# Kernel tuning notes

Measured on AMD Instinct MI355X. Metric: run time of the kernel, lower is better.

The kernel has to match this reference:

```python
import jax, jax.numpy as jnp
import numpy as np

V = 50257  # vocab_size
E = 512    # embed_dim
H = 512    # hidden_dim
N = 32     # batch
T = 128    # sequence length


def setup_inputs() -> dict:
    key = jax.random.key(0)
    ks = jax.random.split(key, 8)
    s = 1.0 / np.sqrt(H)  # PyTorch GRUCell init range
    words = jax.random.randint(ks[0], (N, T), 0, V)
    hidden_state = jnp.zeros((N, H), jnp.float32)
    embed_W = jax.random.uniform(ks[1], (V, E), jnp.float32, -1.0, 1.0)  # init_weights uniform_(-1,1)
    W_ih = jax.random.uniform(ks[2], (3 * H, E), jnp.float32, -s, s)
    W_hh = jax.random.uniform(ks[3], (3 * H, H), jnp.float32, -s, s)
    b_ih = jax.random.uniform(ks[4], (3 * H,), jnp.float32, -s, s)
    b_hh = jax.random.uniform(ks[5], (3 * H,), jnp.float32, -s, s)
    emit_W = jax.random.uniform(ks[6], (V, H), jnp.float32, -1.0, 1.0)
    emit_b = jnp.zeros((V,), jnp.float32)
    return {"words": words, "hidden_state": hidden_state, "embed_W": embed_W,
            "W_ih": W_ih, "W_hh": W_hh, "b_ih": b_ih, "b_hh": b_hh,
            "emit_W": emit_W, "emit_b": emit_b}


def _gru_cell(x, h, W_ih, W_hh, b_ih, b_hh):
    gi = x @ W_ih.T + b_ih          # [N, 3H]
    gh = h @ W_hh.T + b_hh          # [N, 3H]
    i_r, i_z, i_n = jnp.split(gi, 3, axis=-1)
    h_r, h_z, h_n = jnp.split(gh, 3, axis=-1)
    r = jax.nn.sigmoid(i_r + h_r)
    z = jax.nn.sigmoid(i_z + h_z)
    n = jnp.tanh(i_n + r * h_n)
    return (1.0 - z) * n + z * h


def reference(words, hidden_state, embed_W, W_ih, W_hh, b_ih, b_hh, emit_W, emit_b):
    emb = embed_W[words[:, :-1]]        # [N, T-1, E]
    xs = jnp.swapaxes(emb, 0, 1)        # [T-1, N, E]
    targets = words[:, 1:].T            # [T-1, N]

    def step(h, inp):
        x, widx = inp
        h_new = _gru_cell(x, h, W_ih, W_hh, b_ih, b_hh)
        logits = h_new @ emit_W.T + emit_b                 # [N, V]
        logp = jax.nn.log_softmax(logits, axis=-1)
        ll = jnp.take_along_axis(logp, widx[:, None], axis=1)[:, 0]  # [N]
        return h_new, ll

    h_final, lls = jax.lax.scan(step, hidden_state, (xs, targets))
    emit_marginal = lls.sum(axis=0) / (T - 1)              # [N]
    return emit_marginal, h_final
```

## Files before the change

kernel.cpp:

```cpp
#include <hip/hip_runtime.h>
#include <math.h>

#define V_SIZE 50257
#define EMB 512
#define HID 512
#define NB 32
#define TT 128
#define NSTEP 127
#define G3H 1536
#define MROWS 4064
#define MPAD 4096
#define VPAD 50304
#define NT_V 393
#define NBLK_GRU 32
#define NTILE (16 * NT_V)
#define NWORKER 448
#define SMEM_BYTES 77312

typedef __attribute__((ext_vector_type(4))) float f32x4;
typedef __attribute__((ext_vector_type(8))) __bf16 bf16x8;
typedef __attribute__((ext_vector_type(4))) __bf16 bf16x4;

struct u128 { unsigned long long a, b; };

__device__ __forceinline__ void async16(const __bf16* g, __bf16* l) {
    __builtin_amdgcn_global_load_lds(
        (const __attribute__((address_space(1))) void*)g,
        (__attribute__((address_space(3))) void*)l, 16, 0, 0);
}


__global__ void k_prep_emit(const float* __restrict__ src, __bf16* __restrict__ dst) {
    size_t total4 = (size_t)VPAD * 512 / 4;
    size_t real4  = (size_t)V_SIZE * 512 / 4;
    for (size_t i4 = (size_t)blockIdx.x * blockDim.x + threadIdx.x; i4 < total4;
         i4 += (size_t)gridDim.x * blockDim.x) {
        float4 v = (i4 < real4) ? ((const float4*)src)[i4] : make_float4(0.f,0.f,0.f,0.f);
        bf16x4 o = {(__bf16)v.x, (__bf16)v.y, (__bf16)v.z, (__bf16)v.w};
        ((bf16x4*)dst)[i4] = o;
    }
}

__global__ void k_prep_wih(const float* __restrict__ src, __bf16* __restrict__ dst) {
    size_t total4 = (size_t)G3H * 512 / 4;
    for (size_t i4 = (size_t)blockIdx.x * blockDim.x + threadIdx.x; i4 < total4;
         i4 += (size_t)gridDim.x * blockDim.x) {
        float4 v = ((const float4*)src)[i4];
        bf16x4 o = {(__bf16)v.x, (__bf16)v.y, (__bf16)v.z, (__bf16)v.w};
        ((bf16x4*)dst)[i4] = o;
    }
}

__global__ void k_prep_x(const int* __restrict__ words, const float* __restrict__ embed,
                         __bf16* __restrict__ Xb, __bf16* __restrict__ Hs) {
    int s = blockIdx.x;
    int n = blockIdx.y;
    int tid = threadIdx.x;
    if (s < NSTEP) {
        int w = words[n * TT + s];
        size_t row = (size_t)(s * NB + n);
        const float4* src = (const float4*)(embed + (size_t)w * EMB);
        bf16x4* dst = (bf16x4*)(Xb + row * EMB);
        for (int c = tid; c < EMB / 4; c += 128) {
            float4 v = src[c];
            bf16x4 o = {(__bf16)v.x, (__bf16)v.y, (__bf16)v.z, (__bf16)v.w};
            dst[c] = o;
        }
    } else {
        size_t row = (size_t)(MROWS + n);
        bf16x4 z = {(__bf16)0.f, (__bf16)0.f, (__bf16)0.f, (__bf16)0.f};
        for (int c = tid; c < EMB / 4; c += 128) {
            ((bf16x4*)(Xb + row * EMB))[c] = z;
            ((bf16x4*)(Hs + row * HID))[c] = z;
        }
    }
}

__global__ void k_prep_h0(const float* __restrict__ h0, __bf16* __restrict__ Hbuf,
                          int* __restrict__ ctrl) {
    int b = blockIdx.x;
    if (b < NB) {
        for (int k = threadIdx.x; k < HID; k += 256)
            Hbuf[b * HID + k] = (__bf16)h0[b * HID + k];
    } else {
        for (int k = threadIdx.x; k < 2048; k += 256) ctrl[k] = 0;
    }
}


__device__ __forceinline__ void mm128(const __bf16* __restrict__ A,
                                      const __bf16* __restrict__ B,
                                      int mBase, int nBase, f32x4 acc[4][4],
                                      __bf16* As, __bf16* Bs) {
    const int tid = threadIdx.x;
    const int lane = tid & 63, wave = tid >> 6;
    const int wm = wave >> 1, wn = wave & 1;
    const int lane15 = lane & 15, quad = lane >> 4;
    for (int kc = 0; kc < 512; kc += 64) {
        __syncthreads();
#pragma unroll
        for (int i = 0; i < 4; ++i) {
            int c = (wave * 4 + i) * 64 + lane;
            int row = c >> 3, ci = c & 7;
            int cis = ci ^ (row & 7);
            async16(A + (size_t)(mBase + row) * 512 + kc + (cis << 3), As + (wave * 4 + i) * 512);
            async16(B + (size_t)(nBase + row) * 512 + kc + (cis << 3), Bs + (wave * 4 + i) * 512);
        }
        __syncthreads();
#pragma unroll
        for (int ks = 0; ks < 64; ks += 32) {
            bf16x8 a4[4], b4[4];
#pragma unroll
            for (int mi = 0; mi < 4; ++mi) {
                int row = wm * 64 + mi * 16 + lane15;
                int L = (ks >> 3) + quad;
                a4[mi] = *(const bf16x8*)(As + row * 64 + ((L ^ (row & 7)) << 3));
            }
#pragma unroll
            for (int ni = 0; ni < 4; ++ni) {
                int row = wn * 64 + ni * 16 + lane15;
                int L = (ks >> 3) + quad;
                b4[ni] = *(const bf16x8*)(Bs + row * 64 + ((L ^ (row & 7)) << 3));
            }
#pragma unroll
            for (int mi = 0; mi < 4; ++mi)
#pragma unroll
                for (int ni = 0; ni < 4; ++ni)
                    acc[mi][ni] = __builtin_amdgcn_mfma_f32_16x16x32_bf16(
                        a4[mi], b4[ni], acc[mi][ni], 0, 0, 0);
        }
    }
}

__global__ __launch_bounds__(256) void k_gemm_gi(const __bf16* __restrict__ Xb,
                                                 const __bf16* __restrict__ Wihb,
                                                 const float* __restrict__ b_ih,
                                                 const float* __restrict__ b_hh,
                                                 float* __restrict__ gi) {
    __shared__ __align__(16) __bf16 As[128 * 64];
    __shared__ __align__(16) __bf16 Bs[128 * 64];
    f32x4 acc[4][4];
    f32x4 z = {0.f, 0.f, 0.f, 0.f};
#pragma unroll
    for (int mi = 0; mi < 4; ++mi)
#pragma unroll
        for (int ni = 0; ni < 4; ++ni) acc[mi][ni] = z;
    int mBase = blockIdx.x * 128, nBase = blockIdx.y * 128;
    mm128(Xb, Wihb, mBase, nBase, acc, As, Bs);
    const int tid = threadIdx.x, lane = tid & 63, wave = tid >> 6;
    const int wm = wave >> 1, wn = wave & 1, lane15 = lane & 15, quad = lane >> 4;
#pragma unroll
    for (int ni = 0; ni < 4; ++ni) {
        int col = nBase + wn * 64 + ni * 16 + lane15;
        float bias = b_ih[col] + (col < 1024 ? b_hh[col] : 0.0f);
#pragma unroll
        for (int mi = 0; mi < 4; ++mi) {
            int rowb = wm * 64 + mi * 16 + quad * 4;
#pragma unroll
            for (int r = 0; r < 4; ++r) {
                int m = mBase + rowb + r;
                gi[(size_t)m * G3H + col] = acc[mi][ni][r] + bias;
            }
        }
    }
}

#define CREDp(w,g,m,jc) Cred[(((w)*3+(g))*32+(m))*17+(jc)]

__global__ __launch_bounds__(256, 2) void k_fused(
    const float* __restrict__ W_hh, const float* __restrict__ gi,
    const float* __restrict__ b_hh, const float* __restrict__ h0,
    __bf16* __restrict__ Hbuf,
    __bf16* __restrict__ Hs,
    float* __restrict__ Hfin,
    const __bf16* __restrict__ Wemb,
    const float* __restrict__ emit_b,
    float2* __restrict__ partials,
    int* __restrict__ ctrl)
{
    __shared__ __align__(16) char smem[SMEM_BYTES];
    __shared__ int tShare;
    const int tid = threadIdx.x;
    const int lane = tid & 63, wave = tid >> 6;
    const int lane15 = lane & 15, quad = lane >> 4;
    int* ticket = ctrl;
    int* flags  = ctrl + 32;
    int* prog   = ctrl + 64;

    if (blockIdx.x < NBLK_GRU) {
        const int blk = blockIdx.x;
        const int j0 = blk * 16;
        __bf16* Wl  = (__bf16*)smem;
        float* Cred = (float*)(smem + 49920);
        __bf16 (*HbO)[16] = (__bf16(*)[16])(smem + 76032);

        for (int idx = tid; idx < 48 * 128; idx += 256) {
            int rr = idx >> 7, k4 = (idx & 127) << 2;
            int g = rr >> 4, jc = rr & 15;
            float4 v = *(const float4*)(W_hh + (size_t)(g * 512 + j0 + jc) * 512 + k4);
            __bf16* d = &Wl[rr * 520 + k4];
            d[0] = (__bf16)v.x; d[1] = (__bf16)v.y; d[2] = (__bf16)v.z; d[3] = (__bf16)v.w;
        }

        const int m0 = tid >> 4, jc0 = tid & 15;
        const int m1 = m0 + 16;
        const float bhn = b_hh[1024 + j0 + jc0];
        const int k0 = wave * 128;
        float hp0 = h0[(size_t)m0 * HID + j0 + jc0];
        float hp1 = h0[(size_t)m1 * HID + j0 + jc0];

        float ir0, iz0, in0, ir1, iz1, in1;
        {
            const float* g0 = gi + (size_t)m0 * G3H + j0 + jc0;
            const float* g1 = gi + (size_t)m1 * G3H + j0 + jc0;
            ir0 = g0[0]; iz0 = g0[512]; in0 = g0[1024];
            ir1 = g1[0]; iz1 = g1[512]; in1 = g1[1024];
        }
        __syncthreads();

        for (int s = 0; s < NSTEP; ++s) {
            const __bf16* hb = Hbuf + (size_t)(s & 1) * NB * HID;
            unsigned long long hq[2][4][2];
#pragma unroll
            for (int mt = 0; mt < 2; ++mt)
#pragma unroll
                for (int kk = 0; kk < 4; ++kk) {
                    const unsigned long long* pp = (const unsigned long long*)
                        (hb + (size_t)(mt * 16 + lane15) * HID + k0 + kk * 32 + quad * 8);
                    hq[mt][kk][0] = __hip_atomic_load(pp, __ATOMIC_RELAXED, __HIP_MEMORY_SCOPE_AGENT);
                    hq[mt][kk][1] = __hip_atomic_load(pp + 1, __ATOMIC_RELAXED, __HIP_MEMORY_SCOPE_AGENT);
                }

            f32x4 acc[2][3];
            f32x4 zz = {0.f, 0.f, 0.f, 0.f};
#pragma unroll
            for (int mt = 0; mt < 2; ++mt)
#pragma unroll
                for (int g = 0; g < 3; ++g) acc[mt][g] = zz;
#pragma unroll
            for (int kk = 0; kk < 4; ++kk) {
                int ks = kk * 32;
                bf16x8 a0 = __builtin_bit_cast(bf16x8, u128{hq[0][kk][0], hq[0][kk][1]});
                bf16x8 a1 = __builtin_bit_cast(bf16x8, u128{hq[1][kk][0], hq[1][kk][1]});
#pragma unroll
                for (int g = 0; g < 3; ++g) {
                    bf16x8 b4 = *(const bf16x8*)(&Wl[(g * 16 + lane15) * 520 + k0 + ks + quad * 8]);
                    acc[0][g] = __builtin_amdgcn_mfma_f32_16x16x32_bf16(a0, b4, acc[0][g], 0, 0, 0);
                    acc[1][g] = __builtin_amdgcn_mfma_f32_16x16x32_bf16(a1, b4, acc[1][g], 0, 0, 0);
                }
            }
#pragma unroll
            for (int mt = 0; mt < 2; ++mt)
#pragma unroll
                for (int g = 0; g < 3; ++g)
#pragma unroll
                    for (int r = 0; r < 4; ++r)
                        CREDp(wave, g, mt * 16 + quad * 4 + r, lane15) = acc[mt][g][r];
            __syncthreads();

            {
                float gr = CREDp(0,0,m0,jc0) + CREDp(1,0,m0,jc0) + CREDp(2,0,m0,jc0) + CREDp(3,0,m0,jc0);
                float gz = CREDp(0,1,m0,jc0) + CREDp(1,1,m0,jc0) + CREDp(2,1,m0,jc0) + CREDp(3,1,m0,jc0);
                float gn = CREDp(0,2,m0,jc0) + CREDp(1,2,m0,jc0) + CREDp(2,2,m0,jc0) + CREDp(3,2,m0,jc0);
                float r = 1.f / (1.f + expf(-(ir0 + gr)));
                float zg = 1.f / (1.f + expf(-(iz0 + gz)));
                float nn = tanhf(in0 + r * (gn + bhn));
                hp0 = (1.f - zg) * nn + zg * hp0;
                HbO[m0][jc0] = (__bf16)hp0;
            }
            {
                float gr = CREDp(0,0,m1,jc0) + CREDp(1,0,m1,jc0) + CREDp(2,0,m1,jc0) + CREDp(3,0,m1,jc0);
                float gz = CREDp(0,1,m1,jc0) + CREDp(1,1,m1,jc0) + CREDp(2,1,m1,jc0) + CREDp(3,1,m1,jc0);
                float gn = CREDp(0,2,m1,jc0) + CREDp(1,2,m1,jc0) + CREDp(2,2,m1,jc0) + CREDp(3,2,m1,jc0);
                float r = 1.f / (1.f + expf(-(ir1 + gr)));
                float zg = 1.f / (1.f + expf(-(iz1 + gz)));
                float nn = tanhf(in1 + r * (gn + bhn));
                hp1 = (1.f - zg) * nn + zg * hp1;
                HbO[m1][jc0] = (__bf16)hp1;
            }
            __syncthreads();

            if (tid < 128) {
                int m = tid >> 2, g4 = tid & 3;
                unsigned long long v0 = *(const unsigned short*)&HbO[m][g4 * 4 + 0];
                unsigned long long v1 = *(const unsigned short*)&HbO[m][g4 * 4 + 1];
                unsigned long long v2 = *(const unsigned short*)&HbO[m][g4 * 4 + 2];
                unsigned long long v3 = *(const unsigned short*)&HbO[m][g4 * 4 + 3];
                unsigned long long pk = v0 | (v1 << 16) | (v2 << 32) | (v3 << 48);
                unsigned long long* dst = (unsigned long long*)
                    (Hbuf + (size_t)((s + 1) & 1) * NB * HID + (size_t)m * HID + j0 + g4 * 4);
                __hip_atomic_store(dst, pk, __ATOMIC_RELAXED, __HIP_MEMORY_SCOPE_AGENT);
                unsigned long long* dst2 = (unsigned long long*)
                    (Hs + (size_t)(s * NB + m) * HID + j0 + g4 * 4);
                __hip_atomic_store(dst2, pk, __ATOMIC_RELAXED, __HIP_MEMORY_SCOPE_AGENT);
            }

            __builtin_amdgcn_s_waitcnt(0x0f70);
            __syncthreads();

            if (tid == 0)
                __hip_atomic_store(&flags[blk], s + 1,
                                   __ATOMIC_RELAXED, __HIP_MEMORY_SCOPE_AGENT);

            float nir0, niz0, nin0, nir1, niz1, nin1;
            if (s + 1 < NSTEP) {
                const float* g0 = gi + (size_t)((s + 1) * NB + m0) * G3H + j0 + jc0;
                const float* g1 = gi + (size_t)((s + 1) * NB + m1) * G3H + j0 + jc0;
                nir0 = g0[0]; niz0 = g0[512]; nin0 = g0[1024];
                nir1 = g1[0]; niz1 = g1[512]; nin1 = g1[1024];
            } else {
                nir0 = niz0 = nin0 = nir1 = niz1 = nin1 = 0.f;
            }

            if (wave == 0) {
                for (;;) {
                    int f = __hip_atomic_load(&flags[lane & 31], __ATOMIC_RELAXED,
                                              __HIP_MEMORY_SCOPE_AGENT);
                    if (__all(f >= s + 1)) break;
                    __builtin_amdgcn_s_sleep(1);
                }
            }
            __syncthreads();

            if (blk == 0 && tid < 8)
                __hip_atomic_store(&prog[tid << 5], s + 1,
                                   __ATOMIC_RELAXED, __HIP_MEMORY_SCOPE_AGENT);

            ir0 = nir0; iz0 = niz0; in0 = nin0;
            ir1 = nir1; iz1 = niz1; in1 = nin1;
        }

        Hfin[(size_t)m0 * HID + j0 + jc0] = hp0;
        Hfin[(size_t)m1 * HID + j0 + jc0] = hp1;

    } else {
        __bf16* As = (__bf16*)smem;
        __bf16* Bs = (__bf16*)(smem + 32768);
        int* myprog = prog + ((blockIdx.x & 7) << 5);
        const float NINF = -__builtin_inff();

        for (;;) {
            if (tid == 0) {
                int t = __hip_atomic_fetch_add(ticket, 1, __ATOMIC_RELAXED,
                                               __HIP_MEMORY_SCOPE_AGENT);
                tShare = t;
                if (t < NTILE) {
                    int mc = t / NT_V;
                    int need = (mc == 15) ? NSTEP : 8 * (mc + 1);
                    while (__hip_atomic_load(myprog, __ATOMIC_RELAXED,
                                             __HIP_MEMORY_SCOPE_AGENT) < need)
                        __builtin_amdgcn_s_sleep(32);
                }
            }
            __syncthreads();
            int t = tShare;
            if (t >= NTILE) break;
            int mc = t / NT_V;
            int nT = t - mc * NT_V;
            int mBase = mc * 256, nBase = nT * 128;

            f32x4 acc[4][8];
            f32x4 z = {0.f, 0.f, 0.f, 0.f};
#pragma unroll
            for (int mi = 0; mi < 4; ++mi)
#pragma unroll
                for (int ni = 0; ni < 8; ++ni) acc[mi][ni] = z;

            for (int kc = 0; kc < 512; kc += 64) {
                __syncthreads();
#pragma unroll
                for (int i = 0; i < 8; ++i) {
                    int c = (wave * 8 + i) * 64 + lane;
                    int row = c >> 3, ci = c & 7;
                    int cis = ci ^ (row & 7);
                    async16(Hs + (size_t)(mBase + row) * 512 + kc + (cis << 3),
                            As + (wave * 8 + i) * 512);
                }
#pragma unroll
                for (int i = 0; i < 4; ++i) {
                    int c = (wave * 4 + i) * 64 + lane;
                    int row = c >> 3, ci = c & 7;
                    int cis = ci ^ (row & 7);
                    async16(Wemb + (size_t)(nBase + row) * 512 + kc + (cis << 3),
                            Bs + (wave * 4 + i) * 512);
                }
                __syncthreads();
#pragma unroll
                for (int ks = 0; ks < 64; ks += 32) {
                    int L = (ks >> 3) + quad;
                    bf16x8 a4[4], b4[8];
#pragma unroll
                    for (int mi = 0; mi < 4; ++mi) {
                        int row = wave * 64 + mi * 16 + lane15;
                        a4[mi] = *(const bf16x8*)(As + row * 64 + ((L ^ (row & 7)) << 3));
                    }
#pragma unroll
                    for (int ni = 0; ni < 8; ++ni) {
                        int row = ni * 16 + lane15;
                        b4[ni] = *(const bf16x8*)(Bs + row * 64 + ((L ^ (row & 7)) << 3));
                    }
#pragma unroll
                    for (int mi = 0; mi < 4; ++mi)
#pragma unroll
                        for (int ni = 0; ni < 8; ++ni)
                            acc[mi][ni] = __builtin_amdgcn_mfma_f32_16x16x32_bf16(
                                a4[mi], b4[ni], acc[mi][ni], 0, 0, 0);
                }
            }

            float bv[8];
            bool valid[8];
#pragma unroll
            for (int ni = 0; ni < 8; ++ni) {
                int col = nBase + ni * 16 + lane15;
                valid[ni] = (col < V_SIZE);
                bv[ni] = valid[ni] ? emit_b[col] : 0.0f;
            }
#pragma unroll
            for (int mi = 0; mi < 4; ++mi) {
#pragma unroll
                for (int r = 0; r < 4; ++r) {
                    float vals[8];
                    float vmax = NINF;
#pragma unroll
                    for (int ni = 0; ni < 8; ++ni) {
                        float v = acc[mi][ni][r] + bv[ni];
                        if (!valid[ni]) v = NINF;
                        vals[ni] = v;
                        vmax = fmaxf(vmax, v);
                    }
#pragma unroll
                    for (int off = 1; off < 16; off <<= 1)
                        vmax = fmaxf(vmax, __shfl_xor(vmax, off));
                    float ssum = 0.f;
#pragma unroll
                    for (int ni = 0; ni < 8; ++ni) ssum += expf(vals[ni] - vmax);
#pragma unroll
                    for (int off = 1; off < 16; off <<= 1) ssum += __shfl_xor(ssum, off);
                    if (lane15 == 0) {
                        int m = mBase + wave * 64 + mi * 16 + quad * 4 + r;
                        partials[(size_t)m * NT_V + nT] = make_float2(vmax, ssum);
                    }
                }
            }
        }
    }
}

__global__ __launch_bounds__(128) void k_row_ll(const float2* __restrict__ partials,
                                                const __bf16* __restrict__ Hs,
                                                const __bf16* __restrict__ Wemb,
                                                const float* __restrict__ emit_b,
                                                const int* __restrict__ words,
                                                float* __restrict__ lls) {
    int s = blockIdx.x, n = blockIdx.y;
    int m = s * NB + n;
    int tid = threadIdx.x;
    int lane = tid & 63, w = tid >> 6;
    __shared__ float sm[2], ss[2], sd[2];
    const float2* prow = partials + (size_t)m * NT_V;
    float M = -__builtin_inff();
    for (int i = tid; i < NT_V; i += 128) M = fmaxf(M, prow[i].x);
#pragma unroll
    for (int off = 1; off < 64; off <<= 1) M = fmaxf(M, __shfl_xor(M, off));
    if (lane == 0) sm[w] = M;
    __syncthreads();
    M = fmaxf(sm[0], sm[1]);
    float S = 0.f;
    for (int i = tid; i < NT_V; i += 128) {
        float2 p = prow[i];
        S += p.y * expf(p.x - M);
    }
#pragma unroll
    for (int off = 1; off < 64; off <<= 1) S += __shfl_xor(S, off);
    if (lane == 0) ss[w] = S;
    __syncthreads();
    S = ss[0] + ss[1];
    int tw = words[n * TT + s + 1];
    float d = 0.f;
    const __bf16* hr = Hs + (size_t)m * HID;
    const __bf16* wr = Wemb + (size_t)tw * HID;
    for (int k = tid; k < HID; k += 128) d += (float)hr[k] * (float)wr[k];
#pragma unroll
    for (int off = 1; off < 64; off <<= 1) d += __shfl_xor(d, off);
    if (lane == 0) sd[w] = d;
    __syncthreads();
    if (tid == 0) {
        float dt = sd[0] + sd[1];
        lls[m] = dt + emit_b[tw] - (M + logf(S));
    }
}

__global__ __launch_bounds__(128) void k_final(const float* __restrict__ lls,
                                               const float* __restrict__ Hfin,
                                               float* __restrict__ out) {
    int n = blockIdx.x;
    int tid = threadIdx.x;
    float s = 0.f;
    for (int i = tid; i < NSTEP; i += 128) s += lls[i * NB + n];
#pragma unroll
    for (int off = 1; off < 64; off <<= 1) s += __shfl_xor(s, off);
    __shared__ float t2[2];
    if ((tid & 63) == 0) t2[tid >> 6] = s;
    __syncthreads();
    if (tid == 0) out[n] = (t2[0] + t2[1]) / (float)NSTEP;
    for (int i = tid; i < HID; i += 128) out[NB + n * HID + i] = Hfin[(size_t)n * HID + i];
}

extern "C" void kernel_launch(void* const* d_in, const int* in_sizes, int n_in,
                              void* d_out, int out_size, void* d_ws, size_t ws_size,
                              hipStream_t stream) {
    const int*   words   = (const int*)d_in[0];
    const float* hidden0 = (const float*)d_in[1];
    const float* embed_W = (const float*)d_in[2];
    const float* W_ih    = (const float*)d_in[3];
    const float* W_hh    = (const float*)d_in[4];
    const float* b_ih    = (const float*)d_in[5];
    const float* b_hh    = (const float*)d_in[6];
    const float* emit_W  = (const float*)d_in[7];
    const float* emit_b  = (const float*)d_in[8];
    float* out = (float*)d_out;

    char* p = (char*)d_ws;
    auto alloc = [&](size_t bytes) {
        void* r = (void*)p;
        p += (bytes + 255) & ~(size_t)255;
        return r;
    };
    __bf16* emit_Wb = (__bf16*)alloc((size_t)VPAD * 512 * 2);
    __bf16* Xb      = (__bf16*)alloc((size_t)MPAD * 512 * 2);
    __bf16* Wihb    = (__bf16*)alloc((size_t)G3H * 512 * 2);
    float*  gi      = (float*)alloc((size_t)MPAD * G3H * 4);
    __bf16* Hs      = (__bf16*)alloc((size_t)MPAD * 512 * 2);
    __bf16* Hbuf    = (__bf16*)alloc((size_t)2 * NB * HID * 2);
    float*  Hfin    = (float*)alloc((size_t)NB * HID * 4);
    float2* partials= (float2*)alloc((size_t)MPAD * NT_V * 8);
    float*  lls     = (float*)alloc((size_t)MROWS * 4);
    int*    ctrl    = (int*)alloc(2048 * 4);

    k_prep_emit<<<4096, 256, 0, stream>>>(emit_W, emit_Wb);
    k_prep_x<<<dim3(128, 32), 128, 0, stream>>>(words, embed_W, Xb, Hs);
    k_prep_wih<<<768, 256, 0, stream>>>(W_ih, Wihb);
    k_prep_h0<<<NB + 1, 256, 0, stream>>>(hidden0, Hbuf, ctrl);

    k_gemm_gi<<<dim3(32, 12), 256, 0, stream>>>(Xb, Wihb, b_ih, b_hh, gi);

    k_fused<<<NBLK_GRU + NWORKER, 256, 0, stream>>>(
        W_hh, gi, b_hh, hidden0, Hbuf, Hs, Hfin, emit_Wb, emit_b, partials, ctrl);

    k_row_ll<<<dim3(NSTEP, 32), 128, 0, stream>>>(partials, Hs, emit_Wb, emit_b, words, lls);
    k_final<<<32, 128, 0, stream>>>(lls, Hfin, out);
}
```

Before: 898.2 us.

## Merge four prep kernels into one launch and shrink fused worker count

Combines the emit-weight, W_ih, embedding-gather and h0/ctrl prep kernels into a single kernel that dispatches on block index, removing three launches and their serialization gaps. Separately, the number of worker blocks in the fused GRU+emit kernel drops from 448 to 128, which changes how the vocab-tile work is split against the GRU recurrence blocks. Fewer workers may cut contention with the recurrence blocks or the cost of spinning on flags, but gives less parallelism for the large emit GEMM.

After: 1.302 ms. +45.0%, slower.

```diff
diff --git a/kernel.cpp b/kernel.cpp
--- a/kernel.cpp
+++ b/kernel.cpp
@@ -14,7 +14,7 @@
 #define NT_V 393
 #define NBLK_GRU 32
 #define NTILE (16 * NT_V)
-#define NWORKER 448
+#define NWORKER 128
 #define SMEM_BYTES 77312
 
 typedef __attribute__((ext_vector_type(4))) float f32x4;
@@ -29,61 +29,61 @@
         (__attribute__((address_space(3))) void*)l, 16, 0, 0);
 }
 
-
-__global__ void k_prep_emit(const float* __restrict__ src, __bf16* __restrict__ dst) {
-    size_t total4 = (size_t)VPAD * 512 / 4;
-    size_t real4  = (size_t)V_SIZE * 512 / 4;
-    for (size_t i4 = (size_t)blockIdx.x * blockDim.x + threadIdx.x; i4 < total4;
-         i4 += (size_t)gridDim.x * blockDim.x) {
-        float4 v = (i4 < real4) ? ((const float4*)src)[i4] : make_float4(0.f,0.f,0.f,0.f);
+#define PREP_EMIT_BLKS 4096
+#define PREP_WIH_BLKS 768
+#define PREP_X_BLKS 128
+#define PREP_GRID (PREP_EMIT_BLKS + PREP_WIH_BLKS + PREP_X_BLKS + NB + 1)
+
+__global__ __launch_bounds__(256) void k_prep(
+    const int* __restrict__ words, const float* __restrict__ embed,
+    const float* __restrict__ emit_W, const float* __restrict__ W_ih,
+    const float* __restrict__ h0,
+    __bf16* __restrict__ emit_Wb, __bf16* __restrict__ Wihb,
+    __bf16* __restrict__ Xb, __bf16* __restrict__ Hs,
+    __bf16* __restrict__ Hbuf, int* __restrict__ ctrl)
+{
+    int b = blockIdx.x;
+    int tid = threadIdx.x;
+    if (b < PREP_EMIT_BLKS) {
+        size_t total4 = (size_t)VPAD * 512 / 4;
+        size_t real4  = (size_t)V_SIZE * 512 / 4;
+        for (size_t i4 = (size_t)b * 256 + tid; i4 < total4;
+             i4 += (size_t)PREP_EMIT_BLKS * 256) {
+            float4 v = (i4 < real4) ? ((const float4*)emit_W)[i4] : make_float4(0.f,0.f,0.f,0.f);
+            bf16x4 o = {(__bf16)v.x, (__bf16)v.y, (__bf16)v.z, (__bf16)v.w};
+            ((bf16x4*)emit_Wb)[i4] = o;
+        }
+    } else if (b < PREP_EMIT_BLKS + PREP_WIH_BLKS) {
+        size_t i4 = (size_t)(b - PREP_EMIT_BLKS) * 256 + tid;
+        float4 v = ((const float4*)W_ih)[i4];
         bf16x4 o = {(__bf16)v.x, (__bf16)v.y, (__bf16)v.z, (__bf16)v.w};
-        ((bf16x4*)dst)[i4] = o;
-    }
-}
-
-__global__ void k_prep_wih(const float* __restrict__ src, __bf16* __restrict__ dst) {
-    size_t total4 = (size_t)G3H * 512 / 4;
-    for (size_t i4 = (size_t)blockIdx.x * blockDim.x + threadIdx.x; i4 < total4;
-         i4 += (size_t)gridDim.x * blockDim.x) {
-        float4 v = ((const float4*)src)[i4];
-        bf16x4 o = {(__bf16)v.x, (__bf16)v.y, (__bf16)v.z, (__bf16)v.w};
-        ((bf16x4*)dst)[i4] = o;
-    }
-}
-
-__global__ void k_prep_x(const int* __restrict__ words, const float* __restrict__ embed,
-                         __bf16* __restrict__ Xb, __bf16* __restrict__ Hs) {
-    int s = blockIdx.x;
-    int n = blockIdx.y;
-    int tid = threadIdx.x;
-    if (s < NSTEP) {
-        int w = words[n * TT + s];
-        size_t row = (size_t)(s * NB + n);
-        const float4* src = (const float4*)(embed + (size_t)w * EMB);
-        bf16x4* dst = (bf16x4*)(Xb + row * EMB);
-        for (int c = tid; c < EMB / 4; c += 128) {
-            float4 v = src[c];
-            bf16x4 o = {(__bf16)v.x, (__bf16)v.y, (__bf16)v.z, (__bf16)v.w};
-            dst[c] = o;
+        ((bf16x4*)Wihb)[i4] = o;
+    } else if (b < PREP_EMIT_BLKS + PREP_WIH_BLKS + PREP_X_BLKS) {
+        int s = b - (PREP_EMIT_BLKS + PREP_WIH_BLKS);
+        if (s < NSTEP) {
+            for (int idx = tid; idx < 32 * 128; idx += 256) {
+                int n = idx >> 7, c = idx & 127;
+                int w = words[n * TT + s];
+                float4 v = ((const float4*)(embed + (size_t)w * EMB))[c];
+                bf16x4 o = {(__bf16)v.x, (__bf16)v.y, (__bf16)v.z, (__bf16)v.w};
+                ((bf16x4*)(Xb + (size_t)(s * NB + n) * EMB))[c] = o;
+            }
+        } else {
+            bf16x4 z = {(__bf16)0.f, (__bf16)0.f, (__bf16)0.f, (__bf16)0.f};
+            for (int idx = tid; idx < 32 * 128; idx += 256) {
+                int n = idx >> 7, c = idx & 127;
+                ((bf16x4*)(Xb + (size_t)(MROWS + n) * EMB))[c] = z;
+                ((bf16x4*)(Hs + (size_t)(MROWS + n) * HID))[c] = z;
+            }
         }
     } else {
-        size_t row = (size_t)(MROWS + n);
-        bf16x4 z = {(__bf16)0.f, (__bf16)0.f, (__bf16)0.f, (__bf16)0.f};
-        for (int c = tid; c < EMB / 4; c += 128) {
-            ((bf16x4*)(Xb + row * EMB))[c] = z;
-            ((bf16x4*)(Hs + row * HID))[c] = z;
-        }
-    }
-}
-
-__global__ void k_prep_h0(const float* __restrict__ h0, __bf16* __restrict__ Hbuf,
-                          int* __restrict__ ctrl) {
-    int b = blockIdx.x;
-    if (b < NB) {
-        for (int k = threadIdx.x; k < HID; k += 256)
-            Hbuf[b * HID + k] = (__bf16)h0[b * HID + k];
-    } else {
-        for (int k = threadIdx.x; k < 2048; k += 256) ctrl[k] = 0;
+        int b2 = b - (PREP_EMIT_BLKS + PREP_WIH_BLKS + PREP_X_BLKS);
+        if (b2 < NB) {
+            for (int k = tid; k < HID; k += 256)
+                Hbuf[b2 * HID + k] = (__bf16)h0[b2 * HID + k];
+        } else {
+            for (int k = tid; k < 2048; k += 256) ctrl[k] = 0;
+        }
     }
 }
 
@@ -538,10 +538,8 @@
     float*  lls     = (float*)alloc((size_t)MROWS * 4);
     int*    ctrl    = (int*)alloc(2048 * 4);
 
-    k_prep_emit<<<4096, 256, 0, stream>>>(emit_W, emit_Wb);
-    k_prep_x<<<dim3(128, 32), 128, 0, stream>>>(words, embed_W, Xb, Hs);
-    k_prep_wih<<<768, 256, 0, stream>>>(W_ih, Wihb);
-    k_prep_h0<<<NB + 1, 256, 0, stream>>>(hidden0, Hbuf, ctrl);
+    k_prep<<<PREP_GRID, 256, 0, stream>>>(words, embed_W, emit_W, W_ih, hidden0,
+                                          emit_Wb, Wihb, Xb, Hs, Hbuf, ctrl);
 
     k_gemm_gi<<<dim3(32, 12), 256, 0, stream>>>(Xb, Wihb, b_ih, b_hh, gi);
 
```
